# Performance work log

Measured on AMD Instinct MI355X. Metric: run time of the kernel, lower is better.

Reference implementation:

```python
import jax, jax.numpy as jnp
import numpy as np

B, S, D_IN, D = 4, 4096, 768, 64

def setup_inputs() -> dict:
    key = jax.random.key(0)
    kx, kq, kk, kv = jax.random.split(key, 4)
    std = 0.02
    return {
        "x": jax.random.normal(kx, (B, S, D_IN), dtype=jnp.float32),
        "wq": jax.random.normal(kq, (D_IN, D), dtype=jnp.float32) * std,
        "wk": jax.random.normal(kk, (D_IN, D), dtype=jnp.float32) * std,
        "wv": jax.random.normal(kv, (D_IN, D), dtype=jnp.float32) * std,
    }

def reference(x, wq, wk, wv):
    # q,k,v: [B,S,d]
    q = jnp.einsum('bsi,id->bsd', x, wq)
    k = jnp.einsum('bsi,id->bsd', x, wk)
    v = jnp.einsum('bsi,id->bsd', x, wv)
    scale = 1.0 / np.sqrt(q.shape[-1]).astype(np.float32)
    scores = jnp.einsum('bqd,bkd->bqk', q, k) * scale  # [B,S,S]
    attn = jax.nn.softmax(scores, axis=-1)
    return jnp.einsum('bqk,bkd->bqd', attn, v)  # [B,S,d]
```

## Files before the change

kernel.cpp:

```cpp
#include <hip/hip_runtime.h>
#include <hip/hip_bf16.h>

#define B_   4
#define S_   4096
#define DIN  768
#define DH   64

typedef float f32x4 __attribute__((ext_vector_type(4)));
typedef short s16x8 __attribute__((ext_vector_type(8)));
typedef int   i32x4 __attribute__((ext_vector_type(4)));
typedef unsigned short u16;

__device__ __forceinline__ u16 f2bf(float f) {
  union { float f; unsigned int u; } a; a.f = f;
  unsigned int u = a.u;
  unsigned int r = (u + 0x7fffu + ((u >> 16) & 1u)) >> 16;
  return (u16)r;
}

__device__ __forceinline__ unsigned int bfpack2(float a, float b) {
  union { float f; unsigned int u; } ua, ub; ua.f = a; ub.f = b;
  return ((ua.u + 0x8000u) >> 16) | ((ub.u + 0x8000u) & 0xffff0000u);
}

__device__ __forceinline__ s16x8 ld8s(const u16* p) {
  return *reinterpret_cast<const s16x8*>(p);
}

__device__ __forceinline__ s16x8 pack8f(float4 a, float4 b) {
  union { i32x4 i; s16x8 s; } u;
  u.i[0] = (int)bfpack2(a.x, a.y);
  u.i[1] = (int)bfpack2(a.z, a.w);
  u.i[2] = (int)bfpack2(b.x, b.y);
  u.i[3] = (int)bfpack2(b.z, b.w);
  return u.s;
}

#define GLD_LDS(gp, lp) \
  __builtin_amdgcn_global_load_lds((const __attribute__((address_space(1))) void*)(gp), \
                                   (__attribute__((address_space(3))) void*)(lp), 16, 0, 0)

__global__ __launch_bounds__(256) void prep_w(const float* __restrict__ wq,
    const float* __restrict__ wk, const float* __restrict__ wv, u16* __restrict__ wt) {
  __shared__ u16 tl[64 * 65];
  int bid = blockIdx.x;
  int mtx = bid / 12;
  int k0 = (bid % 12) * 64;
  const float* src = (mtx == 0) ? wq : (mtx == 1) ? wk : wv;
  float scale = (mtx == 0) ? 0.125f : 1.0f;
  int t = threadIdx.x;
  int rr = t >> 6, cc = t & 63;
#pragma unroll
  for (int i = 0; i < 16; i++) {
    int kr = i * 4 + rr;
    tl[kr * 65 + cc] = f2bf(src[(size_t)(k0 + kr) * 64 + cc] * scale);
  }
  __syncthreads();
  int nbase = mtx * 64;
#pragma unroll
  for (int i = 0; i < 16; i++) {
    int nl = i * 4 + rr;
    int n = nbase + nl;
    int gr = (cc >> 3) ^ (n & 7);
    wt[(size_t)n * DIN + k0 + gr * 8 + (cc & 7)] = tl[cc * 65 + nl];
  }
}

__global__ __launch_bounds__(256, 4) void qkv_gemm(const float* __restrict__ x,
    const u16* __restrict__ wt, u16* __restrict__ qb, u16* __restrict__ kb,
    u16* __restrict__ vt) {
  __shared__ __align__(16) u16 wl[2][96 * 64];
  int t = threadIdx.x;
  int w = t >> 6, l = t & 63, g = l >> 4, lq = l & 15;
  int wr = w >> 1, wc = w & 1;
  int bc = blockIdx.x & 1;
  int m0 = (blockIdx.x >> 1) * 32;
  int nb = bc * 96;

  const float* xrowp = x + (size_t)(m0 + 16 * wr + lq) * DIN + g * 8;

#pragma unroll
  for (int i = 0; i < 3; i++) {
    int tau = i * 4 + w; int nl = 8 * tau + (l >> 3);
    GLD_LDS(wt + (size_t)(nb + nl) * DIN + (l & 7) * 8, &wl[0][tau * 512]);
  }
  float4 xa = *reinterpret_cast<const float4*>(xrowp);
  float4 xb = *reinterpret_cast<const float4*>(xrowp + 4);
  float4 xc = *reinterpret_cast<const float4*>(xrowp + 32);
  float4 xd = *reinterpret_cast<const float4*>(xrowp + 36);
  s16x8 a0 = pack8f(xa, xb), a1 = pack8f(xc, xd);

  f32x4 acc[3];
#pragma unroll
  for (int i = 0; i < 3; i++) acc[i] = f32x4{0.f, 0.f, 0.f, 0.f};

  asm volatile("s_waitcnt vmcnt(0)" ::: "memory");
  __syncthreads();

#pragma unroll
  for (int ks = 0; ks < 12; ks++) {
    int cur = ks & 1;
    float4 na, nb4, nc, nd;
    if (ks < 11) {
      int k1 = (ks + 1) * 64;
#pragma unroll
      for (int i = 0; i < 3; i++) {
        int tau = i * 4 + w; int nl = 8 * tau + (l >> 3);
        GLD_LDS(wt + (size_t)(nb + nl) * DIN + k1 + (l & 7) * 8, &wl[cur ^ 1][tau * 512]);
      }
      na  = *reinterpret_cast<const float4*>(xrowp + k1);
      nb4 = *reinterpret_cast<const float4*>(xrowp + k1 + 4);
      nc  = *reinterpret_cast<const float4*>(xrowp + k1 + 32);
      nd  = *reinterpret_cast<const float4*>(xrowp + k1 + 36);
    }
#pragma unroll
    for (int nt = 0; nt < 3; nt++) {
      int nl = 48 * wc + nt * 16 + lq;
      s16x8 b0 = ld8s(&wl[cur][nl * 64 + ((g ^ (nl & 7)) * 8)]);
      s16x8 b1 = ld8s(&wl[cur][nl * 64 + (((g + 4) ^ (nl & 7)) * 8)]);
      acc[nt] = __builtin_amdgcn_mfma_f32_16x16x32_bf16(a0, b0, acc[nt], 0, 0, 0);
      acc[nt] = __builtin_amdgcn_mfma_f32_16x16x32_bf16(a1, b1, acc[nt], 0, 0, 0);
    }
    if (ks < 11) {
      a0 = pack8f(na, nb4); a1 = pack8f(nc, nd);
      asm volatile("s_waitcnt vmcnt(0)" ::: "memory");
      __syncthreads();
    }
  }

  int b = m0 >> 12;
  int srow0 = (m0 & (S_ - 1)) + 16 * wr + 4 * g;
#pragma unroll
  for (int nt = 0; nt < 3; nt++) {
    int col = nb + 48 * wc + nt * 16 + lq;
    u16* base; int c;
    if (col < 64)       { base = qb; c = col; }
    else if (col < 128) { base = kb; c = col - 64; }
    else                { base = vt; c = col - 128; }
#pragma unroll
    for (int r = 0; r < 4; r++) {
      int srow = srow0 + r;
      u16 hv = f2bf(acc[nt][r]);
      if (col < 128) {
        int gr = (c >> 3) ^ (srow & 7);
        base[(size_t)(b * S_ + srow) * DH + gr * 8 + (c & 7)] = hv;
      } else {
        int gr = ((srow >> 3) & 7) ^ (c & 7);
        base[(size_t)(b * DH + c) * S_ + (srow & ~63) + gr * 8 + (srow & 7)] = hv;
      }
    }
  }
}

__global__ __launch_bounds__(256, 4) void attn(const u16* __restrict__ qb,
    const u16* __restrict__ kb, const u16* __restrict__ vt,
    float* __restrict__ op, float* __restrict__ lp) {
  __shared__ __align__(16) u16 smem[16384];

  int t = threadIdx.x;
  int w = t >> 6, l = t & 63, g = l >> 4, lq = l & 15;
  int bq = blockIdx.x;
  int ks = bq & 3, qt = (bq >> 2) & 63, b = bq >> 8;
  int q0 = qt * 64;
  int kvbase = ks * 1024;

  int sq = q0 + 16 * w + lq;
  const u16* qrow = qb + (size_t)(b * S_ + sq) * DH;
  s16x8 qa0 = ld8s(qrow + ((g ^ (sq & 7)) * 8));
  s16x8 qa1 = ld8s(qrow + (((g + 4) ^ (sq & 7)) * 8));

  int sA = ((2 * (g & 1)) << 4) | lq;
  int idxA = sA << 2;
  int idxB = idxA + 64;
  bool chi = ((g >> 1) & 1);

  float lrun = 0.f;
  f32x4 acco[4];
#pragma unroll
  for (int nt = 0; nt < 4; nt++) acco[nt] = f32x4{0.f, 0.f, 0.f, 0.f};

  int tau0 = w * 2;
  int srow_st = 8 * tau0 + (l >> 3);
  int gcol = (l & 7) * 8;

  {
    u16* dst = smem;
#pragma unroll
    for (int i = 0; i < 2; i++) {
      int row = srow_st + 8 * i;
      GLD_LDS(kb + (size_t)(b * S_ + kvbase + row) * DH + gcol, &dst[(tau0 + i) * 512]);
      GLD_LDS(vt + (size_t)(b * DH + row) * S_ + kvbase + gcol, &dst[4096 + (tau0 + i) * 512]);
    }
    asm volatile("s_waitcnt vmcnt(0)" ::: "memory");
    __syncthreads();
  }

  const float L2E = 1.44269504f;

  for (int it = 0; it < 16; it++) {
    int cur = it & 1;
    bool more = it < 15;
    if (more) {
      int k1 = kvbase + (it + 1) * 64;
      u16* dst = smem + (cur ^ 1) * 8192;
#pragma unroll
      for (int i = 0; i < 2; i++) {
        int row = srow_st + 8 * i;
        GLD_LDS(kb + (size_t)(b * S_ + k1 + row) * DH + gcol, &dst[(tau0 + i) * 512]);
        GLD_LDS(vt + (size_t)(b * DH + row) * S_ + k1 + gcol, &dst[4096 + (tau0 + i) * 512]);
      }
    }
    const u16* kl = smem + cur * 8192;
    const u16* vl = kl + 4096;

    f32x4 accs[4];
#pragma unroll
    for (int kt = 0; kt < 4; kt++) {
      int krow = kt * 16 + lq;
      s16x8 kf0 = ld8s(&kl[krow * 64 + ((g ^ (krow & 7)) * 8)]);
      s16x8 kf1 = ld8s(&kl[krow * 64 + (((g + 4) ^ (krow & 7)) * 8)]);
      f32x4 c = f32x4{0.f, 0.f, 0.f, 0.f};
      c = __builtin_amdgcn_mfma_f32_16x16x32_bf16(kf0, qa0, c, 0, 0, 0);
      c = __builtin_amdgcn_mfma_f32_16x16x32_bf16(kf1, qa1, c, 0, 0, 0);
      accs[kt] = c;
    }

    float s = 0.f;
#pragma unroll
    for (int kt = 0; kt < 4; kt++) {
#pragma unroll
      for (int r = 0; r < 4; r++) {
        float e = exp2f(accs[kt][r] * L2E);
        accs[kt][r] = e; s += e;
      }
    }
    s += __shfl_xor(s, 16);
    s += __shfl_xor(s, 32);
    lrun += s;

    int pk0 = (int)bfpack2(accs[0][0], accs[0][1]);
    int pk1 = (int)bfpack2(accs[0][2], accs[0][3]);
    int pk2 = (int)bfpack2(accs[1][0], accs[1][1]);
    int pk3 = (int)bfpack2(accs[1][2], accs[1][3]);
    int pk4 = (int)bfpack2(accs[2][0], accs[2][1]);
    int pk5 = (int)bfpack2(accs[2][2], accs[2][3]);
    int pk6 = (int)bfpack2(accs[3][0], accs[3][1]);
    int pk7 = (int)bfpack2(accs[3][2], accs[3][3]);

    int fA0 = __builtin_amdgcn_ds_bpermute(idxA, pk0);
    int fA1 = __builtin_amdgcn_ds_bpermute(idxA, pk1);
    int fA2 = __builtin_amdgcn_ds_bpermute(idxA, pk2);
    int fA3 = __builtin_amdgcn_ds_bpermute(idxA, pk3);
    int fA4 = __builtin_amdgcn_ds_bpermute(idxA, pk4);
    int fA5 = __builtin_amdgcn_ds_bpermute(idxA, pk5);
    int fA6 = __builtin_amdgcn_ds_bpermute(idxA, pk6);
    int fA7 = __builtin_amdgcn_ds_bpermute(idxA, pk7);
    int fB0 = __builtin_amdgcn_ds_bpermute(idxB, pk0);
    int fB1 = __builtin_amdgcn_ds_bpermute(idxB, pk1);
    int fB2 = __builtin_amdgcn_ds_bpermute(idxB, pk2);
    int fB3 = __builtin_amdgcn_ds_bpermute(idxB, pk3);
    int fB4 = __builtin_amdgcn_ds_bpermute(idxB, pk4);
    int fB5 = __builtin_amdgcn_ds_bpermute(idxB, pk5);
    int fB6 = __builtin_amdgcn_ds_bpermute(idxB, pk6);
    int fB7 = __builtin_amdgcn_ds_bpermute(idxB, pk7);

    union { i32x4 i; s16x8 h; } upa0, upa1;
    upa0.i[0] = chi ? fA2 : fA0;  upa0.i[1] = chi ? fA3 : fA1;
    upa0.i[2] = chi ? fB2 : fB0;  upa0.i[3] = chi ? fB3 : fB1;
    upa1.i[0] = chi ? fA6 : fA4;  upa1.i[1] = chi ? fA7 : fA5;
    upa1.i[2] = chi ? fB6 : fB4;  upa1.i[3] = chi ? fB7 : fB5;

#pragma unroll
    for (int nt = 0; nt < 4; nt++) {
      int d = nt * 16 + lq;
      s16x8 vf0 = ld8s(&vl[d * 64 + ((g ^ (d & 7)) * 8)]);
      s16x8 vf1 = ld8s(&vl[d * 64 + (((g + 4) ^ (d & 7)) * 8)]);
      acco[nt] = __builtin_amdgcn_mfma_f32_16x16x32_bf16(upa0.h, vf0, acco[nt], 0, 0, 0);
      acco[nt] = __builtin_amdgcn_mfma_f32_16x16x32_bf16(upa1.h, vf1, acco[nt], 0, 0, 0);
    }
    if (more) {
      asm volatile("s_waitcnt vmcnt(0)" ::: "memory");
      __syncthreads();
    }
  }

  float* ob = op + (size_t)bq * 64 * 64;
#pragma unroll
  for (int nt = 0; nt < 4; nt++)
#pragma unroll
    for (int r = 0; r < 4; r++)
      ob[(16 * w + 4 * g + r) * 64 + nt * 16 + lq] = acco[nt][r];
  if (g == 0) lp[bq * 64 + 16 * w + lq] = lrun;
}

__global__ __launch_bounds__(256) void merge(const float* __restrict__ op,
    const float* __restrict__ lp, float* __restrict__ out) {
  int gid = blockIdx.x * 256 + threadIdx.x;
  int row = gid >> 2, dc = (gid & 3) * 16;
  int rr = row & 63;
  int pidx0 = (row >> 6) * 4;
  float lsum = 0.f;
  float4 acc0 = {0,0,0,0}, acc1 = {0,0,0,0}, acc2 = {0,0,0,0}, acc3 = {0,0,0,0};
#pragma unroll
  for (int p = 0; p < 4; p++) {
    lsum += lp[(pidx0 + p) * 64 + rr];
    const float* basep = op + (((size_t)(pidx0 + p) * 64 + rr) * 64 + dc);
    float4 v0 = *reinterpret_cast<const float4*>(basep);
    float4 v1 = *reinterpret_cast<const float4*>(basep + 4);
    float4 v2 = *reinterpret_cast<const float4*>(basep + 8);
    float4 v3 = *reinterpret_cast<const float4*>(basep + 12);
    acc0.x += v0.x; acc0.y += v0.y; acc0.z += v0.z; acc0.w += v0.w;
    acc1.x += v1.x; acc1.y += v1.y; acc1.z += v1.z; acc1.w += v1.w;
    acc2.x += v2.x; acc2.y += v2.y; acc2.z += v2.z; acc2.w += v2.w;
    acc3.x += v3.x; acc3.y += v3.y; acc3.z += v3.z; acc3.w += v3.w;
  }
  float inv = 1.0f / lsum;
  float* ob = out + (size_t)row * 64 + dc;
  float4 o;
  o.x = acc0.x*inv; o.y = acc0.y*inv; o.z = acc0.z*inv; o.w = acc0.w*inv;
  *reinterpret_cast<float4*>(ob) = o;
  o.x = acc1.x*inv; o.y = acc1.y*inv; o.z = acc1.z*inv; o.w = acc1.w*inv;
  *reinterpret_cast<float4*>(ob + 4) = o;
  o.x = acc2.x*inv; o.y = acc2.y*inv; o.z = acc2.z*inv; o.w = acc2.w*inv;
  *reinterpret_cast<float4*>(ob + 8) = o;
  o.x = acc3.x*inv; o.y = acc3.y*inv; o.z = acc3.z*inv; o.w = acc3.w*inv;
  *reinterpret_cast<float4*>(ob + 12) = o;
}

extern "C" void kernel_launch(void* const* d_in, const int* in_sizes, int n_in,
                              void* d_out, int out_size, void* d_ws, size_t ws_size,
                              hipStream_t stream) {
  const float* x  = (const float*)d_in[0];
  const float* wq = (const float*)d_in[1];
  const float* wk = (const float*)d_in[2];
  const float* wv = (const float*)d_in[3];
  float* out = (float*)d_out;
  char* ws = (char*)d_ws;

  u16* wt = (u16*)(ws);
  u16* qb = (u16*)(ws + 294912);
  u16* kb = (u16*)(ws + 294912 + 2097152);
  u16* vt = (u16*)(ws + 294912 + 2 * 2097152);
  float* op = (float*)(ws + 294912 + 3 * 2097152);
  float* lp = (float*)(ws + 294912 + 3 * 2097152 + 16777216);

  hipLaunchKernelGGL(prep_w,   dim3(36),   dim3(256), 0, stream, wq, wk, wv, wt);
  hipLaunchKernelGGL(qkv_gemm, dim3(1024), dim3(256), 0, stream, x, wt, qb, kb, vt);
  hipLaunchKernelGGL(attn,     dim3(1024), dim3(256), 0, stream, qb, kb, vt, op, lp);
  hipLaunchKernelGGL(merge,    dim3(256),  dim3(256), 0, stream, op, lp, out);
}
```

Before: 161.5 us.

## Fuse split-KV merge into attention via atomic last-block reduction, split KV eight ways

Removes the separate merge kernel. Each query tile now counts finished KV splits with an atomic counter, and the last block to finish reduces the partials and writes the output. The KV split grows from 4 to 8 chunks (2048 blocks), partial outputs are stored as bf16 instead of fp32, and the LDS double buffering is replaced by a single buffer so 8 blocks can fit per CU. Float-to-bf16 packing now uses the hardware v_cvt_pk_bf16_f32 instruction. In exchange, loads are no longer overlapped with compute, bf16 partials lose some precision, and the counters must be zeroed each call inside prep_w.

```diff
diff --git a/kernel.cpp b/kernel.cpp
--- a/kernel.cpp
+++ b/kernel.cpp
@@ -18,9 +18,10 @@
   return (u16)r;
 }
 
-__device__ __forceinline__ unsigned int bfpack2(float a, float b) {
-  union { float f; unsigned int u; } ua, ub; ua.f = a; ub.f = b;
-  return ((ua.u + 0x8000u) >> 16) | ((ub.u + 0x8000u) & 0xffff0000u);
+__device__ __forceinline__ int cvtpk(float lo, float hi) {
+  int r;
+  asm("v_cvt_pk_bf16_f32 %0, %1, %2" : "=v"(r) : "v"(lo), "v"(hi));
+  return r;
 }
 
 __device__ __forceinline__ s16x8 ld8s(const u16* p) {
@@ -29,11 +30,17 @@
 
 __device__ __forceinline__ s16x8 pack8f(float4 a, float4 b) {
   union { i32x4 i; s16x8 s; } u;
-  u.i[0] = (int)bfpack2(a.x, a.y);
-  u.i[1] = (int)bfpack2(a.z, a.w);
-  u.i[2] = (int)bfpack2(b.x, b.y);
-  u.i[3] = (int)bfpack2(b.z, b.w);
+  u.i[0] = cvtpk(a.x, a.y);
+  u.i[1] = cvtpk(a.z, a.w);
+  u.i[2] = cvtpk(b.x, b.y);
+  u.i[3] = cvtpk(b.z, b.w);
   return u.s;
+}
+
+__device__ __forceinline__ float bf2f(short h) {
+  union { unsigned int u; float f; } a;
+  a.u = ((unsigned int)(unsigned short)h) << 16;
+  return a.f;
 }
 
 #define GLD_LDS(gp, lp) \
@@ -41,14 +48,16 @@
                                    (__attribute__((address_space(3))) void*)(lp), 16, 0, 0)
 
 __global__ __launch_bounds__(256) void prep_w(const float* __restrict__ wq,
-    const float* __restrict__ wk, const float* __restrict__ wv, u16* __restrict__ wt) {
+    const float* __restrict__ wk, const float* __restrict__ wv, u16* __restrict__ wt,
+    int* __restrict__ cnt) {
   __shared__ u16 tl[64 * 65];
   int bid = blockIdx.x;
+  int t = threadIdx.x;
+  if (bid == 0) cnt[t] = 0;
   int mtx = bid / 12;
   int k0 = (bid % 12) * 64;
   const float* src = (mtx == 0) ? wq : (mtx == 1) ? wk : wv;
   float scale = (mtx == 0) ? 0.125f : 1.0f;
-  int t = threadIdx.x;
   int rr = t >> 6, cc = t & 63;
 #pragma unroll
   for (int i = 0; i < 16; i++) {
@@ -152,17 +161,19 @@
   }
 }
 
-__global__ __launch_bounds__(256, 4) void attn(const u16* __restrict__ qb,
+__global__ __launch_bounds__(256, 8) void attn(const u16* __restrict__ qb,
     const u16* __restrict__ kb, const u16* __restrict__ vt,
-    float* __restrict__ op, float* __restrict__ lp) {
-  __shared__ __align__(16) u16 smem[16384];
+    u16* __restrict__ op, float* __restrict__ lpv, int* __restrict__ cnt,
+    float* __restrict__ out) {
+  __shared__ __align__(16) u16 smem[8192];
+  __shared__ int is_last;
 
   int t = threadIdx.x;
   int w = t >> 6, l = t & 63, g = l >> 4, lq = l & 15;
   int bq = blockIdx.x;
-  int ks = bq & 3, qt = (bq >> 2) & 63, b = bq >> 8;
+  int ks = bq & 7, qt = (bq >> 3) & 63, b = bq >> 9;
   int q0 = qt * 64;
-  int kvbase = ks * 1024;
+  int kvbase = ks * 512;
 
   int sq = q0 + 16 * w + lq;
   const u16* qrow = qb + (size_t)(b * S_ + sq) * DH;
@@ -183,42 +194,29 @@
   int srow_st = 8 * tau0 + (l >> 3);
   int gcol = (l & 7) * 8;
 
-  {
-    u16* dst = smem;
-#pragma unroll
-    for (int i = 0; i < 2; i++) {
-      int row = srow_st + 8 * i;
-      GLD_LDS(kb + (size_t)(b * S_ + kvbase + row) * DH + gcol, &dst[(tau0 + i) * 512]);
-      GLD_LDS(vt + (size_t)(b * DH + row) * S_ + kvbase + gcol, &dst[4096 + (tau0 + i) * 512]);
-    }
+  const u16* ksrc = kb + (size_t)(b * S_ + kvbase + srow_st) * DH + gcol;
+  const u16* vsrc = vt + (size_t)(b * DH + srow_st) * S_ + kvbase + gcol;
+  u16* kdst = smem + tau0 * 512;
+  u16* vdst = smem + 4096 + tau0 * 512;
+
+  const float L2E = 1.44269504f;
+
+  for (int it = 0; it < 8; it++) {
+    if (it) __syncthreads();
+    GLD_LDS(ksrc, kdst);
+    GLD_LDS(ksrc + 8 * DH, kdst + 512);
+    GLD_LDS(vsrc, vdst);
+    GLD_LDS(vsrc + 8 * S_, vdst + 512);
+    ksrc += 64 * DH; vsrc += 64;
     asm volatile("s_waitcnt vmcnt(0)" ::: "memory");
     __syncthreads();
-  }
-
-  const float L2E = 1.44269504f;
-
-  for (int it = 0; it < 16; it++) {
-    int cur = it & 1;
-    bool more = it < 15;
-    if (more) {
-      int k1 = kvbase + (it + 1) * 64;
-      u16* dst = smem + (cur ^ 1) * 8192;
-#pragma unroll
-      for (int i = 0; i < 2; i++) {
-        int row = srow_st + 8 * i;
-        GLD_LDS(kb + (size_t)(b * S_ + k1 + row) * DH + gcol, &dst[(tau0 + i) * 512]);
-        GLD_LDS(vt + (size_t)(b * DH + row) * S_ + k1 + gcol, &dst[4096 + (tau0 + i) * 512]);
-      }
-    }
-    const u16* kl = smem + cur * 8192;
-    const u16* vl = kl + 4096;
 
     f32x4 accs[4];
 #pragma unroll
     for (int kt = 0; kt < 4; kt++) {
       int krow = kt * 16 + lq;
-      s16x8 kf0 = ld8s(&kl[krow * 64 + ((g ^ (krow & 7)) * 8)]);
-      s16x8 kf1 = ld8s(&kl[krow * 64 + (((g + 4) ^ (krow & 7)) * 8)]);
+      s16x8 kf0 = ld8s(&smem[krow * 64 + ((g ^ (krow & 7)) * 8)]);
+      s16x8 kf1 = ld8s(&smem[krow * 64 + (((g + 4) ^ (krow & 7)) * 8)]);
       f32x4 c = f32x4{0.f, 0.f, 0.f, 0.f};
       c = __builtin_amdgcn_mfma_f32_16x16x32_bf16(kf0, qa0, c, 0, 0, 0);
       c = __builtin_amdgcn_mfma_f32_16x16x32_bf16(kf1, qa1, c, 0, 0, 0);
@@ -238,14 +236,14 @@
     s += __shfl_xor(s, 32);
     lrun += s;
 
-    int pk0 = (int)bfpack2(accs[0][0], accs[0][1]);
-    int pk1 = (int)bfpack2(accs[0][2], accs[0][3]);
-    int pk2 = (int)bfpack2(accs[1][0], accs[1][1]);
-    int pk3 = (int)bfpack2(accs[1][2], accs[1][3]);
-    int pk4 = (int)bfpack2(accs[2][0], accs[2][1]);
-    int pk5 = (int)bfpack2(accs[2][2], accs[2][3]);
-    int pk6 = (int)bfpack2(accs[3][0], accs[3][1]);
-    int pk7 = (int)bfpack2(accs[3][2], accs[3][3]);
+    int pk0 = cvtpk(accs[0][0], accs[0][1]);
+    int pk1 = cvtpk(accs[0][2], accs[0][3]);
+    int pk2 = cvtpk(accs[1][0], accs[1][1]);
+    int pk3 = cvtpk(accs[1][2], accs[1][3]);
+    int pk4 = cvtpk(accs[2][0], accs[2][1]);
+    int pk5 = cvtpk(accs[2][2], accs[2][3]);
+    int pk6 = cvtpk(accs[3][0], accs[3][1]);
+    int pk7 = cvtpk(accs[3][2], accs[3][3]);
 
     int fA0 = __builtin_amdgcn_ds_bpermute(idxA, pk0);
     int fA1 = __builtin_amdgcn_ds_bpermute(idxA, pk1);
@@ -270,6 +268,7 @@
     upa1.i[0] = chi ? fA6 : fA4;  upa1.i[1] = chi ? fA7 : fA5;
     upa1.i[2] = chi ? fB6 : fB4;  upa1.i[3] = chi ? fB7 : fB5;
 
+    const u16* vl = smem + 4096;
 #pragma unroll
     for (int nt = 0; nt < 4; nt++) {
       int d = nt * 16 + lq;
@@ -278,53 +277,49 @@
       acco[nt] = __builtin_amdgcn_mfma_f32_16x16x32_bf16(upa0.h, vf0, acco[nt], 0, 0, 0);
       acco[nt] = __builtin_amdgcn_mfma_f32_16x16x32_bf16(upa1.h, vf1, acco[nt], 0, 0, 0);
     }
-    if (more) {
-      asm volatile("s_waitcnt vmcnt(0)" ::: "memory");
-      __syncthreads();
-    }
-  }
-
-  float* ob = op + (size_t)bq * 64 * 64;
+  }
+
+  u16* ob = op + (size_t)bq * 4096;
 #pragma unroll
   for (int nt = 0; nt < 4; nt++)
 #pragma unroll
     for (int r = 0; r < 4; r++)
-      ob[(16 * w + 4 * g + r) * 64 + nt * 16 + lq] = acco[nt][r];
-  if (g == 0) lp[bq * 64 + 16 * w + lq] = lrun;
-}
-
-__global__ __launch_bounds__(256) void merge(const float* __restrict__ op,
-    const float* __restrict__ lp, float* __restrict__ out) {
-  int gid = blockIdx.x * 256 + threadIdx.x;
-  int row = gid >> 2, dc = (gid & 3) * 16;
-  int rr = row & 63;
-  int pidx0 = (row >> 6) * 4;
-  float lsum = 0.f;
-  float4 acc0 = {0,0,0,0}, acc1 = {0,0,0,0}, acc2 = {0,0,0,0}, acc3 = {0,0,0,0};
-#pragma unroll
-  for (int p = 0; p < 4; p++) {
-    lsum += lp[(pidx0 + p) * 64 + rr];
-    const float* basep = op + (((size_t)(pidx0 + p) * 64 + rr) * 64 + dc);
-    float4 v0 = *reinterpret_cast<const float4*>(basep);
-    float4 v1 = *reinterpret_cast<const float4*>(basep + 4);
-    float4 v2 = *reinterpret_cast<const float4*>(basep + 8);
-    float4 v3 = *reinterpret_cast<const float4*>(basep + 12);
-    acc0.x += v0.x; acc0.y += v0.y; acc0.z += v0.z; acc0.w += v0.w;
-    acc1.x += v1.x; acc1.y += v1.y; acc1.z += v1.z; acc1.w += v1.w;
-    acc2.x += v2.x; acc2.y += v2.y; acc2.z += v2.z; acc2.w += v2.w;
-    acc3.x += v3.x; acc3.y += v3.y; acc3.z += v3.z; acc3.w += v3.w;
-  }
-  float inv = 1.0f / lsum;
-  float* ob = out + (size_t)row * 64 + dc;
-  float4 o;
-  o.x = acc0.x*inv; o.y = acc0.y*inv; o.z = acc0.z*inv; o.w = acc0.w*inv;
-  *reinterpret_cast<float4*>(ob) = o;
-  o.x = acc1.x*inv; o.y = acc1.y*inv; o.z = acc1.z*inv; o.w = acc1.w*inv;
-  *reinterpret_cast<float4*>(ob + 4) = o;
-  o.x = acc2.x*inv; o.y = acc2.y*inv; o.z = acc2.z*inv; o.w = acc2.w*inv;
-  *reinterpret_cast<float4*>(ob + 8) = o;
-  o.x = acc3.x*inv; o.y = acc3.y*inv; o.z = acc3.z*inv; o.w = acc3.w*inv;
-  *reinterpret_cast<float4*>(ob + 12) = o;
+      ob[(16 * w + 4 * g + r) * 64 + nt * 16 + lq] = f2bf(acco[nt][r]);
+  if (g == 0) lpv[bq * 64 + 16 * w + lq] = lrun;
+
+  if (t == 0) {
+    int old = __hip_atomic_fetch_add(&cnt[b * 64 + qt], 1,
+                                     __ATOMIC_ACQ_REL, __HIP_MEMORY_SCOPE_AGENT);
+    is_last = (old == 7);
+  }
+  __syncthreads();
+  if (is_last) {
+    __builtin_amdgcn_fence(__ATOMIC_ACQUIRE, "agent");
+    int row = t >> 2, dc = (t & 3) * 16;
+    const u16* obase = op + ((size_t)(b * 64 + qt) * 8) * 4096 + row * 64 + dc;
+    const float* lbase = lpv + (b * 64 + qt) * 8 * 64 + row;
+    float lsum = 0.f;
+    float a[16];
+#pragma unroll
+    for (int j = 0; j < 16; j++) a[j] = 0.f;
+#pragma unroll
+    for (int p = 0; p < 8; p++) {
+      lsum += lbase[p * 64];
+      s16x8 v0 = ld8s(obase + p * 4096);
+      s16x8 v1 = ld8s(obase + p * 4096 + 8);
+#pragma unroll
+      for (int j = 0; j < 8; j++) { a[j] += bf2f(v0[j]); a[8 + j] += bf2f(v1[j]); }
+    }
+    float inv = 1.0f / lsum;
+    float* od = out + (size_t)(b * S_ + q0 + row) * DH + dc;
+#pragma unroll
+    for (int j4 = 0; j4 < 4; j4++) {
+      float4 o;
+      o.x = a[j4 * 4 + 0] * inv; o.y = a[j4 * 4 + 1] * inv;
+      o.z = a[j4 * 4 + 2] * inv; o.w = a[j4 * 4 + 3] * inv;
+      *reinterpret_cast<float4*>(od + j4 * 4) = o;
+    }
+  }
 }
 
 extern "C" void kernel_launch(void* const* d_in, const int* in_sizes, int n_in,
@@ -341,11 +336,11 @@
   u16* qb = (u16*)(ws + 294912);
   u16* kb = (u16*)(ws + 294912 + 2097152);
   u16* vt = (u16*)(ws + 294912 + 2 * 2097152);
-  float* op = (float*)(ws + 294912 + 3 * 2097152);
-  float* lp = (float*)(ws + 294912 + 3 * 2097152 + 16777216);
-
-  hipLaunchKernelGGL(prep_w,   dim3(36),   dim3(256), 0, stream, wq, wk, wv, wt);
+  u16* op = (u16*)(ws + 294912 + 3 * 2097152);
+  float* lpv = (float*)(ws + 294912 + 3 * 2097152 + 16777216);
+  int* cnt = (int*)(ws + 294912 + 3 * 2097152 + 16777216 + 524288);
+
+  hipLaunchKernelGGL(prep_w,   dim3(36),   dim3(256), 0, stream, wq, wk, wv, wt, cnt);
   hipLaunchKernelGGL(qkv_gemm, dim3(1024), dim3(256), 0, stream, x, wt, qb, kb, vt);
-  hipLaunchKernelGGL(attn,     dim3(1024), dim3(256), 0, stream, qb, kb, vt, op, lp);
-  hipLaunchKernelGGL(merge,    dim3(256),  dim3(256), 0, stream, op, lp, out);
-}
+  hipLaunchKernelGGL(attn,     dim3(2048), dim3(256), 0, stream, qb, kb, vt, op, lpv, cnt, out);
+}
```

Measured after the change: 248.4 us. 53.8% more time.
